# Kernel tuning notes

Hardware: AMD Instinct MI355X
Metric: run time of the kernel (lower is better)

## Reference

```python
import jax, jax.numpy as jnp
import numpy as np

B, S, D, H = 4, 512, 768, 200


def setup_inputs() -> dict:
    key = jax.random.key(0)
    ks = jax.random.split(key, 6)
    x = jax.random.normal(ks[0], (B, S, D), dtype=jnp.float32)
    # Linear default init ~ U(-1/sqrt(fan_in), 1/sqrt(fan_in)); scaled normal is fine for a baseline
    W_head = jax.random.normal(ks[1], (D, H), dtype=jnp.float32) * (1.0 / np.sqrt(D))
    b_head = jnp.zeros((H,), dtype=jnp.float32)
    W_tail = jax.random.normal(ks[2], (D, H), dtype=jnp.float32) * (1.0 / np.sqrt(D))
    b_tail = jnp.zeros((H,), dtype=jnp.float32)
    # xavier_normal on [200,200,200]: fan_in = fan_out = 200*200 -> std = sqrt(2/80000)
    U = jax.random.normal(ks[3], (H, H, H), dtype=jnp.float32) * np.sqrt(2.0 / (2 * H * H))
    W_down = jax.random.normal(ks[4], (H, 1), dtype=jnp.float32) * (1.0 / np.sqrt(H))
    b_down = jnp.zeros((1,), dtype=jnp.float32)
    return {"x": x, "W_head": W_head, "b_head": b_head, "W_tail": W_tail,
            "b_tail": b_tail, "U": U, "W_down": W_down, "b_down": b_down}


def reference(x, W_head, b_head, W_tail, b_tail, U, W_down, b_down):
    # head/tail projections with ReLU: [B,S,H]
    head = jax.nn.relu(x @ W_head + b_head)
    tail = jax.nn.relu(x @ W_tail + b_tail)
    # biaffine: 'bxi,oij,byj->bxyo' done as two contractions
    tmp = jnp.einsum('bxi,oij->bxoj', head, U)            # [B,S,H,H]
    logits = jnp.einsum('bxoj,byj->bxyo', tmp, tail)       # [B,S,S,H] (== permuted boxy)
    # down_layer(200->1).squeeze(-1); rope branch in source is dead (rope_logits = 0)
    scores = (logits @ W_down)[..., 0] + b_down[0]         # [B,S,S]
    return scores / jnp.sqrt(jnp.asarray(200.0, dtype=scores.dtype))
```

## Files before the change

kernel.cpp:

```cpp
#include <hip/hip_runtime.h>

#define H 200
#define D 768
#define BATCH 4
#define S 512
#define M (BATCH*S)
#define KP 224
#define NP 208
#define NCAT 400
#define NC4 (H*H/4)
#define VT_BLOCKS 313
#define PROJ_BLOCKS 400
#define PAD_BLOCKS 32
#define K2_BLOCKS (VT_BLOCKS + PROJ_BLOCKS + PAD_BLOCKS)
#define PREP_BLOCKS 512

typedef __attribute__((ext_vector_type(8))) short bf16x8;
typedef __attribute__((ext_vector_type(4))) float f32x4;
typedef unsigned short us;

__device__ inline us f2bf(float f) {
    union { float f; unsigned u; } v; v.f = f;
    return (us)((v.u + 0x7FFF + ((v.u >> 16) & 1)) >> 16);
}

__global__ __launch_bounds__(256) void prep_lite(
        const float* __restrict__ x,  const float* __restrict__ Wh,
        const float* __restrict__ Wt,
        us* __restrict__ xb, us* __restrict__ Wcb) {
    const int GTH = PREP_BLOCKS * 256;
    int gtid = blockIdx.x * 256 + threadIdx.x;
    {
        const float4* x4 = (const float4*)x;
        ushort4* xb4 = (ushort4*)xb;
        for (int t = gtid; t < M * D / 4; t += GTH) {
            float4 v = x4[t];
            ushort4 o; o.x = f2bf(v.x); o.y = f2bf(v.y); o.z = f2bf(v.z); o.w = f2bf(v.w);
            xb4[t] = o;
        }
    }
    for (int id = gtid; id < NCAT * D; id += GTH) {
        int n = id / D, k = id % D;
        float v = (n < H) ? Wh[k * H + n] : Wt[k * H + (n - H)];
        Wcb[id] = f2bf(v);
    }
}

__global__ __launch_bounds__(256) void projvt(
        const float* __restrict__ U,  const float* __restrict__ Wd,
        const us* __restrict__ xb,    const us* __restrict__ Wcb,
        const float* __restrict__ bh, const float* __restrict__ bt,
        us* __restrict__ VTb, us* __restrict__ headb, us* __restrict__ tailb,
        us* __restrict__ hvb) {
    int bid = blockIdx.x;
    if (bid < VT_BLOCKS) {
        __shared__ float4 red[8][32];
        int cl = threadIdx.x & 31, q = threadIdx.x >> 5;
        int c = bid * 32 + cl;
        const float4* U4 = (const float4*)U;
        float4 acc = make_float4(0.f, 0.f, 0.f, 0.f);
        if (c < NC4) {
            int o0 = q * 25;
            #pragma unroll
            for (int o = o0; o < o0 + 25; ++o) {
                float w = Wd[o];
                float4 u = U4[(size_t)o * NC4 + c];
                acc.x += w * u.x; acc.y += w * u.y;
                acc.z += w * u.z; acc.w += w * u.w;
            }
        }
        red[q][cl] = acc;
        __syncthreads();
        if (q == 0 && c < NC4) {
            #pragma unroll
            for (int g = 1; g < 8; ++g) {
                float4 r = red[g][cl];
                acc.x += r.x; acc.y += r.y; acc.z += r.z; acc.w += r.w;
            }
            int i = c / (H / 4), j0 = (c % (H / 4)) * 4;
            VTb[(j0 + 0) * KP + i] = f2bf(acc.x);
            VTb[(j0 + 1) * KP + i] = f2bf(acc.y);
            VTb[(j0 + 2) * KP + i] = f2bf(acc.z);
            VTb[(j0 + 3) * KP + i] = f2bf(acc.w);
        }
        return;
    }
    bid -= VT_BLOCKS;
    if (bid < PROJ_BLOCKS) {
        int w = threadIdx.x >> 6, lane = threadIdx.x & 63;
        int t = bid * 4 + w;
        int quad = lane >> 4, col = lane & 15;
        int m0 = (t & 63) * 32, n0 = (t >> 6) * 16;
        const bf16x8* A0 = (const bf16x8*)(xb + (m0 + col) * D + quad * 8);
        const bf16x8* A1 = (const bf16x8*)(xb + (m0 + 16 + col) * D + quad * 8);
        const bf16x8* Bp = (const bf16x8*)(Wcb + (n0 + col) * D + quad * 8);
        f32x4 acc0 = {0.f,0.f,0.f,0.f}, acc1 = {0.f,0.f,0.f,0.f};
        #pragma unroll 4
        for (int kk = 0; kk < D / 32; ++kk) {
            bf16x8 a0 = A0[kk * 4];
            bf16x8 a1 = A1[kk * 4];
            bf16x8 b  = Bp[kk * 4];
            acc0 = __builtin_amdgcn_mfma_f32_16x16x32_bf16(a0, b, acc0, 0, 0, 0);
            acc1 = __builtin_amdgcn_mfma_f32_16x16x32_bf16(a1, b, acc1, 0, 0, 0);
        }
        int n = n0 + col;
        bool ish = (n < H);
        float bias = ish ? bh[n] : bt[n - H];
        us* dst = ish ? headb : tailb;
        int nn = ish ? n : n - H;
        #pragma unroll
        for (int r = 0; r < 4; ++r) {
            int ma = m0 + quad * 4 + r;
            dst[ma * KP + nn]        = f2bf(fmaxf(acc0[r] + bias, 0.f));
            dst[(ma + 16) * KP + nn] = f2bf(fmaxf(acc1[r] + bias, 0.f));
        }
        return;
    }
    bid -= PROJ_BLOCKS;
    const int GTH = PAD_BLOCKS * 256;
    int gtid = bid * 256 + threadIdx.x;
    for (int id = gtid; id < M * (KP - H); id += GTH) {
        int r = id / (KP - H), c = H + id % (KP - H);
        headb[r * KP + c] = 0; tailb[r * KP + c] = 0;
    }
    for (int id = gtid; id < M * (KP - NP); id += GTH) {
        int r = id / (KP - NP), c = NP + id % (KP - NP);
        hvb[r * KP + c] = 0;
    }
    for (int id = gtid; id < H * (KP - H); id += GTH) {
        int n = id / (KP - H), k = H + id % (KP - H);
        VTb[n * KP + k] = 0;
    }
    for (int id = gtid; id < (NP - H) * KP; id += GTH) {
        int n = H + id / KP, k = id % KP;
        VTb[n * KP + k] = 0;
    }
}

__global__ __launch_bounds__(64) void hv_mfma(
        const us* __restrict__ headb, const us* __restrict__ VTb,
        us* __restrict__ hvb) {
    int lane = threadIdx.x, quad = lane >> 4, col = lane & 15;
    int m0 = blockIdx.x * 32, n0 = blockIdx.y * 16;
    const bf16x8* A0 = (const bf16x8*)(headb + (m0 + col) * KP + quad * 8);
    const bf16x8* A1 = (const bf16x8*)(headb + (m0 + 16 + col) * KP + quad * 8);
    const bf16x8* Bp = (const bf16x8*)(VTb + (n0 + col) * KP + quad * 8);
    f32x4 acc0 = {0.f,0.f,0.f,0.f}, acc1 = {0.f,0.f,0.f,0.f};
    #pragma unroll
    for (int kk = 0; kk < KP / 32; ++kk) {
        bf16x8 a0 = A0[kk * 4];
        bf16x8 a1 = A1[kk * 4];
        bf16x8 b  = Bp[kk * 4];
        acc0 = __builtin_amdgcn_mfma_f32_16x16x32_bf16(a0, b, acc0, 0, 0, 0);
        acc1 = __builtin_amdgcn_mfma_f32_16x16x32_bf16(a1, b, acc1, 0, 0, 0);
    }
    int n = n0 + col;
    #pragma unroll
    for (int r = 0; r < 4; ++r) {
        int ma = m0 + quad * 4 + r;
        hvb[ma * KP + n]        = f2bf(acc0[r]);
        hvb[(ma + 16) * KP + n] = f2bf(acc1[r]);
    }
}

__global__ __launch_bounds__(64) void scores_mfma(
        const us* __restrict__ hvb, const us* __restrict__ tailb,
        const float* __restrict__ bd, float* __restrict__ out) {
    int lane = threadIdx.x, quad = lane >> 4, col = lane & 15;
    int b = blockIdx.z;
    int m0 = blockIdx.x * 32, n0 = blockIdx.y * 32;
    const us* A  = hvb   + (size_t)b * S * KP;
    const us* Bm = tailb + (size_t)b * S * KP;
    const bf16x8* A0 = (const bf16x8*)(A  + (m0 + col) * KP + quad * 8);
    const bf16x8* A1 = (const bf16x8*)(A  + (m0 + 16 + col) * KP + quad * 8);
    const bf16x8* B0 = (const bf16x8*)(Bm + (n0 + col) * KP + quad * 8);
    const bf16x8* B1 = (const bf16x8*)(Bm + (n0 + 16 + col) * KP + quad * 8);
    f32x4 a00 = {0.f,0.f,0.f,0.f}, a01 = {0.f,0.f,0.f,0.f};
    f32x4 a10 = {0.f,0.f,0.f,0.f}, a11 = {0.f,0.f,0.f,0.f};
    #pragma unroll
    for (int kk = 0; kk < KP / 32; ++kk) {
        bf16x8 a0 = A0[kk * 4];
        bf16x8 a1 = A1[kk * 4];
        bf16x8 b0 = B0[kk * 4];
        bf16x8 b1 = B1[kk * 4];
        a00 = __builtin_amdgcn_mfma_f32_16x16x32_bf16(a0, b0, a00, 0, 0, 0);
        a01 = __builtin_amdgcn_mfma_f32_16x16x32_bf16(a0, b1, a01, 0, 0, 0);
        a10 = __builtin_amdgcn_mfma_f32_16x16x32_bf16(a1, b0, a10, 0, 0, 0);
        a11 = __builtin_amdgcn_mfma_f32_16x16x32_bf16(a1, b1, a11, 0, 0, 0);
    }
    float bias = bd[0];
    const float scale = 0.07071067811865475f;
    float* outb = out + (size_t)b * S * S;
    #pragma unroll
    for (int r = 0; r < 4; ++r) {
        int ma = m0 + quad * 4 + r, mb = ma + 16;
        outb[ma * S + n0 + col]      = (a00[r] + bias) * scale;
        outb[ma * S + n0 + 16 + col] = (a01[r] + bias) * scale;
        outb[mb * S + n0 + col]      = (a10[r] + bias) * scale;
        outb[mb * S + n0 + 16 + col] = (a11[r] + bias) * scale;
    }
}

extern "C" void kernel_launch(void* const* d_in, const int* in_sizes, int n_in,
                              void* d_out, int out_size, void* d_ws, size_t ws_size,
                              hipStream_t stream) {
    const float* x  = (const float*)d_in[0];
    const float* Wh = (const float*)d_in[1];
    const float* bh = (const float*)d_in[2];
    const float* Wt = (const float*)d_in[3];
    const float* bt = (const float*)d_in[4];
    const float* U  = (const float*)d_in[5];
    const float* Wd = (const float*)d_in[6];
    const float* bd = (const float*)d_in[7];
    float* out = (float*)d_out;

    us* xb    = (us*)d_ws;
    us* Wcb   = xb    + (size_t)M * D;
    us* VTb   = Wcb   + (size_t)NCAT * D;
    us* hvb   = VTb   + (size_t)NP * KP;
    us* headb = hvb   + (size_t)M * KP;
    us* tailb = headb + (size_t)M * KP;

    prep_lite<<<PREP_BLOCKS, 256, 0, stream>>>(x, Wh, Wt, xb, Wcb);
    projvt<<<K2_BLOCKS, 256, 0, stream>>>(U, Wd, xb, Wcb, bh, bt,
                                          VTb, headb, tailb, hvb);
    hv_mfma<<<dim3(M / 32, NP / 16), 64, 0, stream>>>(headb, VTb, hvb);
    scores_mfma<<<dim3(S / 32, S / 32, BATCH), 64, 0, stream>>>(hvb, tailb, bd, out);
}
```

Measured before the change: 117.2 us.

## Fuse hv GEMM into scores kernel with swizzled LDS staging

Merges the head·V GEMM and the scores GEMM into one kernel. Each block computes its 32-row hv tile into swizzled shared memory, then four waves compute the 32x128 output slab from it. This removes a launch and the global hv buffer write/read plus its padding zeroing. The cost is that each hv tile is recomputed by the four y-blocks sharing the same rows.

```diff
diff --git a/kernel.cpp b/kernel.cpp
--- a/kernel.cpp
+++ b/kernel.cpp
@@ -14,6 +14,7 @@
 #define PAD_BLOCKS 32
 #define K2_BLOCKS (VT_BLOCKS + PROJ_BLOCKS + PAD_BLOCKS)
 #define PREP_BLOCKS 512
+#define HLDSB 512
 
 typedef __attribute__((ext_vector_type(8))) short bf16x8;
 typedef __attribute__((ext_vector_type(4))) float f32x4;
@@ -22,6 +23,10 @@
 __device__ inline us f2bf(float f) {
     union { float f; unsigned u; } v; v.f = f;
     return (us)((v.u + 0x7FFF + ((v.u >> 16) & 1)) >> 16);
+}
+
+__device__ inline int swzb(int row, int bIR) {
+    return row * HLDSB + ((((bIR >> 4) ^ (row & 7)) << 4) | (bIR & 15));
 }
 
 __global__ __launch_bounds__(256) void prep_lite(
@@ -50,8 +55,7 @@
         const float* __restrict__ U,  const float* __restrict__ Wd,
         const us* __restrict__ xb,    const us* __restrict__ Wcb,
         const float* __restrict__ bh, const float* __restrict__ bt,
-        us* __restrict__ VTb, us* __restrict__ headb, us* __restrict__ tailb,
-        us* __restrict__ hvb) {
+        us* __restrict__ VTb, us* __restrict__ headb, us* __restrict__ tailb) {
     int bid = blockIdx.x;
     if (bid < VT_BLOCKS) {
         __shared__ float4 red[8][32];
@@ -123,10 +127,6 @@
         int r = id / (KP - H), c = H + id % (KP - H);
         headb[r * KP + c] = 0; tailb[r * KP + c] = 0;
     }
-    for (int id = gtid; id < M * (KP - NP); id += GTH) {
-        int r = id / (KP - NP), c = NP + id % (KP - NP);
-        hvb[r * KP + c] = 0;
-    }
     for (int id = gtid; id < H * (KP - H); id += GTH) {
         int n = id / (KP - H), k = H + id % (KP - H);
         VTb[n * KP + k] = 0;
@@ -137,50 +137,59 @@
     }
 }
 
-__global__ __launch_bounds__(64) void hv_mfma(
-        const us* __restrict__ headb, const us* __restrict__ VTb,
-        us* __restrict__ hvb) {
-    int lane = threadIdx.x, quad = lane >> 4, col = lane & 15;
-    int m0 = blockIdx.x * 32, n0 = blockIdx.y * 16;
-    const bf16x8* A0 = (const bf16x8*)(headb + (m0 + col) * KP + quad * 8);
-    const bf16x8* A1 = (const bf16x8*)(headb + (m0 + 16 + col) * KP + quad * 8);
-    const bf16x8* Bp = (const bf16x8*)(VTb + (n0 + col) * KP + quad * 8);
-    f32x4 acc0 = {0.f,0.f,0.f,0.f}, acc1 = {0.f,0.f,0.f,0.f};
-    #pragma unroll
-    for (int kk = 0; kk < KP / 32; ++kk) {
-        bf16x8 a0 = A0[kk * 4];
-        bf16x8 a1 = A1[kk * 4];
-        bf16x8 b  = Bp[kk * 4];
-        acc0 = __builtin_amdgcn_mfma_f32_16x16x32_bf16(a0, b, acc0, 0, 0, 0);
-        acc1 = __builtin_amdgcn_mfma_f32_16x16x32_bf16(a1, b, acc1, 0, 0, 0);
-    }
-    int n = n0 + col;
-    #pragma unroll
-    for (int r = 0; r < 4; ++r) {
-        int ma = m0 + quad * 4 + r;
-        hvb[ma * KP + n]        = f2bf(acc0[r]);
-        hvb[(ma + 16) * KP + n] = f2bf(acc1[r]);
-    }
-}
-
-__global__ __launch_bounds__(64) void scores_mfma(
-        const us* __restrict__ hvb, const us* __restrict__ tailb,
-        const float* __restrict__ bd, float* __restrict__ out) {
-    int lane = threadIdx.x, quad = lane >> 4, col = lane & 15;
-    int b = blockIdx.z;
-    int m0 = blockIdx.x * 32, n0 = blockIdx.y * 32;
-    const us* A  = hvb   + (size_t)b * S * KP;
-    const us* Bm = tailb + (size_t)b * S * KP;
-    const bf16x8* A0 = (const bf16x8*)(A  + (m0 + col) * KP + quad * 8);
-    const bf16x8* A1 = (const bf16x8*)(A  + (m0 + 16 + col) * KP + quad * 8);
-    const bf16x8* B0 = (const bf16x8*)(Bm + (n0 + col) * KP + quad * 8);
-    const bf16x8* B1 = (const bf16x8*)(Bm + (n0 + 16 + col) * KP + quad * 8);
+__global__ __launch_bounds__(256) void hvscores(
+        const us* __restrict__ headb, const us* __restrict__ tailb,
+        const us* __restrict__ VTb,   const float* __restrict__ bd,
+        float* __restrict__ out) {
+    __shared__ us hvs[32 * HLDSB / 2];
+    int w = threadIdx.x >> 6, lane = threadIdx.x & 63;
+    int quad = lane >> 4, col = lane & 15;
+    int mt = blockIdx.x;
+    int b = mt >> 4;
+    int m0 = mt * 32;
+    char* hv8 = (char*)hvs;
+
+    if (threadIdx.x < 64) {
+        int row = threadIdx.x >> 1, ch = 26 + (threadIdx.x & 1);
+        *(uint4*)(hv8 + row * HLDSB + ((ch ^ (row & 7)) << 4)) =
+            make_uint4(0u, 0u, 0u, 0u);
+    }
+
+    for (int nt = w; nt < 13; nt += 4) {
+        int n0 = nt * 16;
+        const bf16x8* A0 = (const bf16x8*)(headb + (m0 + col) * KP + quad * 8);
+        const bf16x8* A1 = (const bf16x8*)(headb + (m0 + 16 + col) * KP + quad * 8);
+        const bf16x8* Bp = (const bf16x8*)(VTb + (n0 + col) * KP + quad * 8);
+        f32x4 acc0 = {0.f,0.f,0.f,0.f}, acc1 = {0.f,0.f,0.f,0.f};
+        #pragma unroll
+        for (int kk = 0; kk < KP / 32; ++kk) {
+            bf16x8 a0 = A0[kk * 4];
+            bf16x8 a1 = A1[kk * 4];
+            bf16x8 bb = Bp[kk * 4];
+            acc0 = __builtin_amdgcn_mfma_f32_16x16x32_bf16(a0, bb, acc0, 0, 0, 0);
+            acc1 = __builtin_amdgcn_mfma_f32_16x16x32_bf16(a1, bb, acc1, 0, 0, 0);
+        }
+        int n = n0 + col;
+        #pragma unroll
+        for (int r = 0; r < 4; ++r) {
+            int row0 = quad * 4 + r;
+            *(us*)(hv8 + swzb(row0, n * 2))      = f2bf(acc0[r]);
+            *(us*)(hv8 + swzb(row0 + 16, n * 2)) = f2bf(acc1[r]);
+        }
+    }
+    __syncthreads();
+
+    int y0 = blockIdx.y * 128 + w * 32;
+    const us* Bm = tailb + ((size_t)b * S + y0) * KP;
+    const bf16x8* B0 = (const bf16x8*)(Bm + col * KP + quad * 8);
+    const bf16x8* B1 = (const bf16x8*)(Bm + (16 + col) * KP + quad * 8);
     f32x4 a00 = {0.f,0.f,0.f,0.f}, a01 = {0.f,0.f,0.f,0.f};
     f32x4 a10 = {0.f,0.f,0.f,0.f}, a11 = {0.f,0.f,0.f,0.f};
     #pragma unroll
     for (int kk = 0; kk < KP / 32; ++kk) {
-        bf16x8 a0 = A0[kk * 4];
-        bf16x8 a1 = A1[kk * 4];
+        int bIR = kk * 64 + quad * 16;
+        bf16x8 a0 = *(const bf16x8*)(hv8 + swzb(col, bIR));
+        bf16x8 a1 = *(const bf16x8*)(hv8 + swzb(col + 16, bIR));
         bf16x8 b0 = B0[kk * 4];
         bf16x8 b1 = B1[kk * 4];
         a00 = __builtin_amdgcn_mfma_f32_16x16x32_bf16(a0, b0, a00, 0, 0, 0);
@@ -190,14 +199,15 @@
     }
     float bias = bd[0];
     const float scale = 0.07071067811865475f;
+    int mloc = (mt & 15) * 32;
     float* outb = out + (size_t)b * S * S;
     #pragma unroll
     for (int r = 0; r < 4; ++r) {
-        int ma = m0 + quad * 4 + r, mb = ma + 16;
-        outb[ma * S + n0 + col]      = (a00[r] + bias) * scale;
-        outb[ma * S + n0 + 16 + col] = (a01[r] + bias) * scale;
-        outb[mb * S + n0 + col]      = (a10[r] + bias) * scale;
-        outb[mb * S + n0 + 16 + col] = (a11[r] + bias) * scale;
+        int ma = mloc + quad * 4 + r, mb = ma + 16;
+        outb[ma * S + y0 + col]      = (a00[r] + bias) * scale;
+        outb[ma * S + y0 + 16 + col] = (a01[r] + bias) * scale;
+        outb[mb * S + y0 + col]      = (a10[r] + bias) * scale;
+        outb[mb * S + y0 + 16 + col] = (a11[r] + bias) * scale;
     }
 }
 
@@ -217,13 +227,11 @@
     us* xb    = (us*)d_ws;
     us* Wcb   = xb    + (size_t)M * D;
     us* VTb   = Wcb   + (size_t)NCAT * D;
-    us* hvb   = VTb   + (size_t)NP * KP;
-    us* headb = hvb   + (size_t)M * KP;
+    us* headb = VTb   + (size_t)NP * KP;
     us* tailb = headb + (size_t)M * KP;
 
     prep_lite<<<PREP_BLOCKS, 256, 0, stream>>>(x, Wh, Wt, xb, Wcb);
     projvt<<<K2_BLOCKS, 256, 0, stream>>>(U, Wd, xb, Wcb, bh, bt,
-                                          VTb, headb, tailb, hvb);
-    hv_mfma<<<dim3(M / 32, NP / 16), 64, 0, stream>>>(headb, VTb, hvb);
-    scores_mfma<<<dim3(S / 32, S / 32, BATCH), 64, 0, stream>>>(hvb, tailb, bd, out);
-}
+                                          VTb, headb, tailb);
+    hvscores<<<dim3(64, 4), 256, 0, stream>>>(headb, tailb, VTb, bd, out);
+}
```

Result: slower. 120.9 us (+3.1%).
